# Optimization experiments

Measured on AMD Instinct MI355X. Metric: run time of the kernel, lower is better.

Reference implementation:

```python
import math
import jax, jax.numpy as jnp
import numpy as np

B, S, H = 2, 2048, 1024
NH = 16
HD = H // NH            # 64
ROT = int(HD * 0.25)    # 16
QKV_SLOTS = 1024
PROJ_SLOTS = 1024
FFN_SLOTS = 4096
EPS = 1e-5


def gelu_l2_norm(x, axis=-1):
    # F.gelu (exact erf) then L2-normalize and rescale by sqrt(dim)
    g = jax.nn.gelu(x, approximate=False)
    n = jnp.linalg.norm(g, ord=2, axis=axis, keepdims=True)
    return g / n * math.sqrt(g.shape[axis])


def layer_norm(x, w, b):
    mu = jnp.mean(x, axis=-1, keepdims=True)
    var = jnp.mean(jnp.square(x - mu), axis=-1, keepdims=True)
    return (x - mu) * jax.lax.rsqrt(var + EPS) * w + b


def pattention(x, key_tok, val_tok):
    # [.., in] @ [slots, in]^T -> [.., slots]; NOTE: scale MULTIPLIES (as in source)
    aw = jnp.einsum('bsh,ph->bsp', x, key_tok) * math.sqrt(x.shape[-1])
    aw = gelu_l2_norm(aw, axis=-1)
    return jnp.einsum('bsp,pd->bsd', aw, val_tok)


def rotary_cos_sin(seq_len, rot_dim, base=10000.0):
    inv_freq = 1.0 / (base ** (jnp.arange(0, rot_dim, 2, dtype=jnp.float32) / rot_dim))
    t = jnp.arange(seq_len, dtype=jnp.float32)
    freqs = jnp.einsum('s,d->sd', t, inv_freq)           # [S, rot/2]
    emb = jnp.concatenate([freqs, freqs], axis=-1)       # [S, rot]
    return jnp.cos(emb), jnp.sin(emb)


def rotate_half(x):
    x1, x2 = jnp.split(x, 2, axis=-1)
    return jnp.concatenate([-x2, x1], axis=-1)


def setup_inputs() -> dict:
    key = jax.random.key(0)
    ks = jax.random.split(key, 12)
    p = lambda k, shape: jax.random.normal(k, shape, dtype=jnp.float32) * 0.02
    return {
        'x': jax.random.normal(ks[0], (B, S, H), dtype=jnp.float32),
        'ln1_w': jnp.ones((H,), jnp.float32), 'ln1_b': jnp.zeros((H,), jnp.float32),
        'ln2_w': jnp.ones((H,), jnp.float32), 'ln2_b': jnp.zeros((H,), jnp.float32),
        'q_key': p(ks[1], (QKV_SLOTS, H)), 'q_val': p(ks[2], (QKV_SLOTS, H)),
        'k_key': p(ks[3], (QKV_SLOTS, H)), 'k_val': p(ks[4], (QKV_SLOTS, H)),
        'v_key': p(ks[5], (QKV_SLOTS, H)), 'v_val': p(ks[6], (QKV_SLOTS, H)),
        'proj_key': p(ks[7], (PROJ_SLOTS, H)), 'proj_val': p(ks[8], (PROJ_SLOTS, H)),
        'ffn_key': p(ks[9], (FFN_SLOTS, H)), 'ffn_val': p(ks[10], (FFN_SLOTS, H)),
    }


def reference(x, ln1_w, ln1_b, ln2_w, ln2_b, q_key, q_val, k_key, k_val,
              v_key, v_val, proj_key, proj_val, ffn_key, ffn_val):
    residual = x
    xn = layer_norm(x, ln1_w, ln1_b)
    q = pattention(xn, q_key, q_val).reshape(B, S, NH, HD)
    k = pattention(xn, k_key, k_val).reshape(B, S, NH, HD)
    v = pattention(xn, v_key, v_val).reshape(B, S, NH, HD)

    cos, sin = rotary_cos_sin(S, ROT)          # [S, ROT]
    cos = cos[None, :, None, :]
    sin = sin[None, :, None, :]
    q_rot, q_pass = q[..., :ROT], q[..., ROT:]
    k_rot, k_pass = k[..., :ROT], k[..., ROT:]
    q_rot = q_rot * cos + rotate_half(q_rot) * sin
    k_rot = k_rot * cos + rotate_half(k_rot) * sin
    q = jnp.concatenate([q_rot, q_pass], axis=-1).transpose(0, 2, 1, 3)  # [B,NH,S,HD]
    k = jnp.concatenate([k_rot, k_pass], axis=-1).transpose(0, 2, 1, 3)
    v = v.transpose(0, 2, 1, 3)

    scale = math.sqrt(HD)
    causal = jnp.triu(jnp.ones((S, S), dtype=bool), k=1)
    attn_mask = jnp.where(causal, jnp.float32(-10000.0), jnp.float32(0.0))
    aw = jnp.einsum('bhqd,bhkd->bhqk', q, k) / scale + attn_mask
    aw = gelu_l2_norm(aw, axis=-1)
    o = jnp.einsum('bhqk,bhkd->bhqd', aw, v)
    o = o.transpose(0, 2, 1, 3).reshape(B, S, H)

    x = residual + pattention(o, proj_key, proj_val)
    residual = x
    x = residual + pattention(layer_norm(x, ln2_w, ln2_b), ffn_key, ffn_val)
    return x
```

## Files before the change

kernel.cpp:

```cpp
#include <hip/hip_runtime.h>

typedef __bf16 bf16x8 __attribute__((ext_vector_type(8)));
typedef float f32x4 __attribute__((ext_vector_type(4)));
typedef unsigned short u16;

__device__ __forceinline__ float b2f(u16 u) {
  union { unsigned int i; float f; } v; v.i = ((unsigned int)u) << 16; return v.f;
}
__device__ __forceinline__ u16 f2b(float f) {
  union { float f; unsigned int i; } v; v.f = f;
  unsigned int x = v.i;
  x += 0x7fffu + ((x >> 16) & 1u);
  return (u16)(x >> 16);
}
__device__ __forceinline__ float gelu_f(float x) {
  float x2 = x * x;
  float p = x * (1.5957691216f + 0.0713548162f * x2);
  float e = __expf(p);
  float r = __builtin_amdgcn_rcpf(1.0f + e);
  return x - x * r;
}
__device__ __forceinline__ void async16(const u16* g, u16* l) {
  __builtin_amdgcn_global_load_lds(
      (const __attribute__((address_space(1))) void*)g,
      (__attribute__((address_space(3))) void*)l, 16, 0, 0);
}
__device__ __forceinline__ void swz(int& bn, int& bm, int& bz) {
  int gx = (int)gridDim.x, gy = (int)gridDim.y;
  int flat = (int)(blockIdx.x + gridDim.x * (blockIdx.y + gridDim.y * blockIdx.z));
  int seq = flat >> 3;
  int nbm = gy >> 3;
  bm = (flat & 7) * nbm + seq % nbm;
  int rest = seq / nbm;
  bn = rest % gx;
  bz = rest / gx;
}

union U4 { uint4 u; u16 s[8]; };

__global__ __launch_bounds__(256) void zero_kernel(float* __restrict__ p, int n) {
  int i = blockIdx.x * 256 + threadIdx.x;
  if (i < n) p[i] = 0.f;
}

__global__ __launch_bounds__(256) void cvt8_kernel(
    const float* __restrict__ qk, const float* __restrict__ kk,
    const float* __restrict__ vk, const float* __restrict__ pk,
    const float* __restrict__ fk, u16* __restrict__ w) {
  int z = blockIdx.y;
  const float* in = (z == 0) ? qk : (z == 1) ? kk : (z == 2) ? vk : (z == 3) ? pk
                    : fk + (size_t)(z - 4) * 4194304 / 4 * 4;
  if (z >= 4) in = fk + (size_t)(z - 4) * 1048576 * 4 / 4;
  in = (z == 0) ? qk : (z == 1) ? kk : (z == 2) ? vk : (z == 3) ? pk
       : fk + (size_t)(z - 4) * 1048576;
  u16* o = w + (size_t)z * 1048576;
  int i = blockIdx.x * 256 + threadIdx.x;
  float4 f = ((const float4*)in)[i];
  ushort4 s;
  s.x = f2b(f.x); s.y = f2b(f.y); s.z = f2b(f.z); s.w = f2b(f.w);
  ((ushort4*)o)[i] = s;
}

__global__ __launch_bounds__(256) void cvtT_kernel(const float* __restrict__ in,
                                                   u16* __restrict__ out, int R, int Cn) {
  __shared__ float t[32][33];
  int bc = blockIdx.x, br = blockIdx.y;
  int tid = threadIdx.x;
  int r = tid >> 5, c = tid & 31;
  #pragma unroll
  for (int i = 0; i < 4; ++i)
    t[r + i * 8][c] = in[(size_t)(br * 32 + r + i * 8) * Cn + bc * 32 + c];
  __syncthreads();
  #pragma unroll
  for (int i = 0; i < 4; ++i)
    out[(size_t)(bc * 32 + r + i * 8) * R + br * 32 + c] = f2b(t[c][r + i * 8]);
}
__global__ __launch_bounds__(256) void cvtT4_kernel(
    const float* __restrict__ a, const float* __restrict__ b,
    const float* __restrict__ c, const float* __restrict__ d,
    u16* __restrict__ out) {
  __shared__ float t[32][33];
  int z = blockIdx.z;
  const float* in = (z == 0) ? a : (z == 1) ? b : (z == 2) ? c : d;
  u16* o = out + (size_t)z * 1048576;
  int bc = blockIdx.x, br = blockIdx.y;
  int tid = threadIdx.x;
  int r = tid >> 5, cc = tid & 31;
  #pragma unroll
  for (int i = 0; i < 4; ++i)
    t[r + i * 8][cc] = in[(size_t)(br * 32 + r + i * 8) * 1024 + bc * 32 + cc];
  __syncthreads();
  #pragma unroll
  for (int i = 0; i < 4; ++i)
    o[(size_t)(bc * 32 + r + i * 8) * 1024 + br * 32 + cc] = f2b(t[cc][r + i * 8]);
}

__global__ __launch_bounds__(256) void ln_kernel(const float* __restrict__ x,
    const float* __restrict__ w, const float* __restrict__ b, u16* __restrict__ out) {
  int wv = threadIdx.x >> 6, lane = threadIdx.x & 63;
  int row = blockIdx.x * 4 + wv;
  const float* xr = x + (size_t)row * 1024;
  float4 v[4];
  float s = 0.f, s2 = 0.f;
  #pragma unroll
  for (int i = 0; i < 4; ++i) {
    v[i] = ((const float4*)xr)[lane + 64 * i];
    s += v[i].x + v[i].y + v[i].z + v[i].w;
    s2 += v[i].x * v[i].x + v[i].y * v[i].y + v[i].z * v[i].z + v[i].w * v[i].w;
  }
  #pragma unroll
  for (int m = 1; m < 64; m <<= 1) { s += __shfl_xor(s, m); s2 += __shfl_xor(s2, m); }
  float mu = s * (1.0f / 1024.0f);
  float inv = rsqrtf(s2 * (1.0f / 1024.0f) - mu * mu + 1e-5f);
  u16* orow = out + (size_t)row * 1024;
  #pragma unroll
  for (int i = 0; i < 4; ++i) {
    int c = (lane + 64 * i) * 4;
    ushort4 o;
    o.x = f2b((v[i].x - mu) * inv * w[c]     + b[c]);
    o.y = f2b((v[i].y - mu) * inv * w[c + 1] + b[c + 1]);
    o.z = f2b((v[i].z - mu) * inv * w[c + 2] + b[c + 2]);
    o.w = f2b((v[i].w - mu) * inv * w[c + 3] + b[c + 3]);
    ((ushort4*)orow)[lane + 64 * i] = o;
  }
}

template <int TM>
__global__ __launch_bounds__(256) void gemm_key(
    const u16* __restrict__ A, size_t sAz,
    const u16* __restrict__ B, size_t sBz,
    u16* __restrict__ C, size_t sCz,
    float* __restrict__ ssqb, size_t sSz,
    int N, int K, float alpha) {
  constexpr int AI = TM / 32;
  __shared__ __align__(16) u16 As[2][TM * 32];
  __shared__ __align__(16) u16 Bs[2][128 * 32];
  int bn, bm, bz;
  swz(bn, bm, bz);
  const u16* Ab = A + (size_t)bz * sAz + (size_t)bm * TM * K;
  const u16* Bb = B + (size_t)bz * sBz + (size_t)bn * 128 * K;
  int tid = threadIdx.x, lane = tid & 63, wv = tid >> 6;
  int quad = lane >> 4, l16 = lane & 15;
  int lr = lane >> 2, lc = (lane & 3) * 8;
  int wm = wv >> 1, wn = wv & 1;
  int RB = wm * (TM / 2), CB = wn * 64;
  f32x4 zero = {0.f, 0.f, 0.f, 0.f};
  f32x4 acc[AI][4];
  #pragma unroll
  for (int i = 0; i < AI; ++i)
    #pragma unroll
    for (int j = 0; j < 4; ++j) acc[i][j] = zero;
  #pragma unroll
  for (int t = 0; t < TM / 64; ++t) {
    int ia = wv * (TM / 64) + t;
    async16(Ab + (size_t)(ia * 16 + lr) * K + lc, &As[0][ia * 512]);
  }
  #pragma unroll
  for (int t = 0; t < 2; ++t) {
    int ib = wv * 2 + t;
    async16(Bb + (size_t)(ib * 16 + lr) * K + lc, &Bs[0][ib * 512]);
  }
  for (int k0 = 0, cur = 0; k0 < K; k0 += 32, cur ^= 1) {
    __syncthreads();
    if (k0 + 32 < K) {
      #pragma unroll
      for (int t = 0; t < TM / 64; ++t) {
        int ia = wv * (TM / 64) + t;
        async16(Ab + (size_t)(ia * 16 + lr) * K + k0 + 32 + lc, &As[cur ^ 1][ia * 512]);
      }
      #pragma unroll
      for (int t = 0; t < 2; ++t) {
        int ib = wv * 2 + t;
        async16(Bb + (size_t)(ib * 16 + lr) * K + k0 + 32 + lc, &Bs[cur ^ 1][ib * 512]);
      }
    }
    bf16x8 af[AI], bf[4];
    #pragma unroll
    for (int i = 0; i < AI; ++i)
      af[i] = *(const bf16x8*)&As[cur][(RB + i * 16 + l16) * 32 + quad * 8];
    #pragma unroll
    for (int j = 0; j < 4; ++j)
      bf[j] = *(const bf16x8*)&Bs[cur][(CB + j * 16 + l16) * 32 + quad * 8];
    #pragma unroll
    for (int i = 0; i < AI; ++i)
      #pragma unroll
      for (int j = 0; j < 4; ++j)
        acc[i][j] = __builtin_amdgcn_mfma_f32_16x16x32_bf16(af[i], bf[j], acc[i][j], 0, 0, 0);
  }
  #pragma unroll
  for (int i = 0; i < AI; ++i) {
    int rbase = bm * TM + RB + i * 16 + quad * 4;
    float srow[4] = {0.f, 0.f, 0.f, 0.f};
    #pragma unroll
    for (int j = 0; j < 4; ++j) {
      int c = bn * 128 + CB + j * 16 + l16;
      #pragma unroll
      for (int reg = 0; reg < 4; ++reg) {
        float g = gelu_f(acc[i][j][reg] * alpha);
        srow[reg] += g * g;
        C[(size_t)bz * sCz + (size_t)(rbase + reg) * N + c] = f2b(g);
      }
    }
    #pragma unroll
    for (int reg = 0; reg < 4; ++reg) {
      float s = srow[reg];
      s += __shfl_xor(s, 1); s += __shfl_xor(s, 2);
      s += __shfl_xor(s, 4); s += __shfl_xor(s, 8);
      if (l16 == 0) atomicAdd(&ssqb[bz * sSz + rbase + reg], s);
    }
  }
}

template <int TM, int MODE>
__global__ __launch_bounds__(256) void gemm_val(
    const u16* __restrict__ A, size_t sAz,
    const u16* __restrict__ B, size_t sBz,
    void* __restrict__ C, size_t sCz,
    const float* __restrict__ ssqb, size_t sSz,
    int N, int K, int kzs, int klen, float sqrtP, const float* __restrict__ res) {
  constexpr int AI = TM / 32;
  __shared__ __align__(16) u16 As[2][TM * 32];
  __shared__ __align__(16) u16 Bs[2][128 * 32];
  int bn, bm, bz;
  swz(bn, bm, bz);
  const u16* Ab = A + (size_t)bz * sAz + (size_t)bm * TM * K;
  const u16* Bb = B + (size_t)bz * sBz + (size_t)bn * 128 * K;
  int tid = threadIdx.x, lane = tid & 63, wv = tid >> 6;
  int quad = lane >> 4, l16 = lane & 15;
  int lr = lane >> 2, lc = (lane & 3) * 8;
  int wm = wv >> 1, wn = wv & 1;
  int RB = wm * (TM / 2), CB = wn * 64;
  f32x4 zero = {0.f, 0.f, 0.f, 0.f};
  f32x4 acc[AI][4];
  #pragma unroll
  for (int i = 0; i < AI; ++i)
    #pragma unroll
    for (int j = 0; j < 4; ++j) acc[i][j] = zero;
  int kb0 = bz * kzs;
  #pragma unroll
  for (int t = 0; t < TM / 64; ++t) {
    int ia = wv * (TM / 64) + t;
    async16(Ab + (size_t)(ia * 16 + lr) * K + kb0 + lc, &As[0][ia * 512]);
  }
  #pragma unroll
  for (int t = 0; t < 2; ++t) {
    int ib = wv * 2 + t;
    async16(Bb + (size_t)(ib * 16 + lr) * K + kb0 + lc, &Bs[0][ib * 512]);
  }
  for (int k0 = kb0, cur = 0; k0 < kb0 + klen; k0 += 32, cur ^= 1) {
    __syncthreads();
    if (k0 + 32 < kb0 + klen) {
      #pragma unroll
      for (int t = 0; t < TM / 64; ++t) {
        int ia = wv * (TM / 64) + t;
        async16(Ab + (size_t)(ia * 16 + lr) * K + k0 + 32 + lc, &As[cur ^ 1][ia * 512]);
      }
      #pragma unroll
      for (int t = 0; t < 2; ++t) {
        int ib = wv * 2 + t;
        async16(Bb + (size_t)(ib * 16 + lr) * K + k0 + 32 + lc, &Bs[cur ^ 1][ib * 512]);
      }
    }
    bf16x8 af[AI], bf[4];
    #pragma unroll
    for (int i = 0; i < AI; ++i)
      af[i] = *(const bf16x8*)&As[cur][(RB + i * 16 + l16) * 32 + quad * 8];
    #pragma unroll
    for (int j = 0; j < 4; ++j)
      bf[j] = *(const bf16x8*)&Bs[cur][(CB + j * 16 + l16) * 32 + quad * 8];
    #pragma unroll
    for (int i = 0; i < AI; ++i)
      #pragma unroll
      for (int j = 0; j < 4; ++j)
        acc[i][j] = __builtin_amdgcn_mfma_f32_16x16x32_bf16(af[i], bf[j], acc[i][j], 0, 0, 0);
  }
  #pragma unroll
  for (int i = 0; i < AI; ++i) {
    int rbase = bm * TM + RB + i * 16 + quad * 4;
    float sc[4];
    if (MODE < 2) {
      #pragma unroll
      for (int reg = 0; reg < 4; ++reg)
        sc[reg] = sqrtP * rsqrtf(ssqb[bz * sSz + rbase + reg]);
    }
    #pragma unroll
    for (int j = 0; j < 4; ++j) {
      int c = bn * 128 + CB + j * 16 + l16;
      #pragma unroll
      for (int reg = 0; reg < 4; ++reg) {
        float v = acc[i][j][reg];
        size_t idx = (size_t)(rbase + reg) * N + c;
        if (MODE == 0) {
          ((u16*)C)[(size_t)bz * sCz + idx] = f2b(v * sc[reg]);
        } else if (MODE == 1) {
          ((float*)C)[idx] = v * sc[reg] + res[idx];
        } else {
          ((float*)C)[(size_t)bz * sCz + idx] = v;
        }
      }
    }
  }
}

__global__ __launch_bounds__(256) void rotary_kernel(u16* __restrict__ qb, u16* __restrict__ kb) {
  const float F[8] = {1.f, 0.31622776601683794f, 0.1f, 0.03162277660168379f,
                      0.01f, 0.0031622776601683794f, 0.001f, 0.00031622776601683794f};
  int t = blockIdx.x * 256 + threadIdx.x;
  int m = t >> 4;
  int h = t & 15;
  int s = m & 2047;
  u16* qp = qb + (size_t)m * 1024 + h * 64;
  u16* kp = kb + (size_t)m * 1024 + h * 64;
  float q[16], k[16];
  #pragma unroll
  for (int d = 0; d < 16; ++d) { q[d] = b2f(qp[d]); k[d] = b2f(kp[d]); }
  #pragma unroll
  for (int i = 0; i < 8; ++i) {
    float ang = (float)s * F[i];
    float c = cosf(ang), sn = sinf(ang);
    qp[i]     = f2b(q[i] * c - q[i + 8] * sn);
    qp[i + 8] = f2b(q[i + 8] * c + q[i] * sn);
    kp[i]     = f2b(k[i] * c - k[i + 8] * sn);
    kp[i + 8] = f2b(k[i + 8] * c + k[i] * sn);
  }
}

__global__ __launch_bounds__(256) void vt_kernel(const u16* __restrict__ vb,
                                                 u16* __restrict__ vT) {
  __shared__ __align__(16) u16 T[64][72];
  int st = blockIdx.x, bh = blockIdx.y;
  int b = bh >> 4, h = bh & 15;
  int tid = threadIdx.x;
  #pragma unroll
  for (int i = 0; i < 2; ++i) {
    int l = tid + 256 * i;
    int s = l >> 3, dc = l & 7;
    *(uint4*)&T[s][dc * 8] =
        *(const uint4*)(vb + (size_t)(b * 2048 + st * 64 + s) * 1024 + h * 64 + dc * 8);
  }
  __syncthreads();
  #pragma unroll
  for (int i = 0; i < 2; ++i) {
    int l = tid + 256 * i;
    int d = l >> 3, scid = l & 7;
    U4 u;
    #pragma unroll
    for (int j = 0; j < 8; ++j) u.s[j] = T[scid * 8 + j][d];
    *(uint4*)(vT + ((size_t)bh * 64 + d) * 2048 + st * 64 + scid * 8) = u.u;
  }
}

__global__ __launch_bounds__(256) void attn_kernel(
    const u16* __restrict__ qb, const u16* __restrict__ kb,
    const u16* __restrict__ vT, u16* __restrict__ ob) {
  __shared__ __align__(16) u16 Qs[64 * 64];
  __shared__ __align__(16) u16 Ks[2][64 * 64];
  __shared__ __align__(16) u16 Vts[2][64 * 64];
  __shared__ __align__(16) u16 Sg[64 * 72];
  int bh = blockIdx.x;
  int qt = 31 - (int)blockIdx.y;
  int b = bh >> 4, h = bh & 15;
  const u16* qp = qb + (size_t)b * 2048 * 1024 + h * 64;
  const u16* kp = kb + (size_t)b * 2048 * 1024 + h * 64;
  const u16* vp = vT + (size_t)bh * 64 * 2048;
  int tid = threadIdx.x, lane = tid & 63, wv = tid >> 6;
  int quad = lane >> 4, l16 = lane & 15;
  int lr8 = lane >> 3, lc8 = (lane & 7) * 8;
  int MR = wv * 16;
  int nkt = qt + 1;
  #pragma unroll
  for (int t = 0; t < 2; ++t) {
    int idx = wv * 2 + t;
    async16(qp + (size_t)(qt * 64 + idx * 8 + lr8) * 1024 + lc8, &Qs[idx * 512]);
    async16(kp + (size_t)(idx * 8 + lr8) * 1024 + lc8, &Ks[0][idx * 512]);
    async16(vp + (size_t)(idx * 8 + lr8) * 2048 + lc8, &Vts[0][idx * 512]);
  }
  f32x4 zero = {0.f, 0.f, 0.f, 0.f};
  f32x4 oacc[4];
  float ssqr[4] = {0.f, 0.f, 0.f, 0.f};
  #pragma unroll
  for (int dn = 0; dn < 4; ++dn) oacc[dn] = zero;
  for (int kt = 0, cur = 0; kt < nkt; ++kt, cur ^= 1) {
    __syncthreads();
    if (kt + 1 < nkt) {
      #pragma unroll
      for (int t = 0; t < 2; ++t) {
        int idx = wv * 2 + t;
        async16(kp + (size_t)((kt + 1) * 64 + idx * 8 + lr8) * 1024 + lc8, &Ks[cur ^ 1][idx * 512]);
        async16(vp + (size_t)(idx * 8 + lr8) * 2048 + (kt + 1) * 64 + lc8, &Vts[cur ^ 1][idx * 512]);
      }
    }
    bf16x8 a0 = *(const bf16x8*)&Qs[(MR + l16) * 64 + quad * 8];
    bf16x8 a1 = *(const bf16x8*)&Qs[(MR + l16) * 64 + 32 + quad * 8];
    bool dg = (kt == qt);
    #pragma unroll
    for (int sn = 0; sn < 4; ++sn) {
      bf16x8 b0 = *(const bf16x8*)&Ks[cur][(sn * 16 + l16) * 64 + quad * 8];
      bf16x8 b1 = *(const bf16x8*)&Ks[cur][(sn * 16 + l16) * 64 + 32 + quad * 8];
      f32x4 s = zero;
      s = __builtin_amdgcn_mfma_f32_16x16x32_bf16(a0, b0, s, 0, 0, 0);
      s = __builtin_amdgcn_mfma_f32_16x16x32_bf16(a1, b1, s, 0, 0, 0);
      int srow = MR + quad * 4;
      int kcol = sn * 16 + l16;
      #pragma unroll
      for (int reg = 0; reg < 4; ++reg) {
        float gl = gelu_f(s[reg] * 0.125f);
        if (dg && kcol > srow + reg) gl = 0.f;
        ssqr[reg] += gl * gl;
        Sg[(srow + reg) * 72 + kcol] = f2b(gl);
      }
    }
    bf16x8 p0 = *(const bf16x8*)&Sg[(MR + l16) * 72 + quad * 8];
    bf16x8 p1 = *(const bf16x8*)&Sg[(MR + l16) * 72 + 32 + quad * 8];
    #pragma unroll
    for (int dn = 0; dn < 4; ++dn) {
      bf16x8 v0 = *(const bf16x8*)&Vts[cur][(dn * 16 + l16) * 64 + quad * 8];
      bf16x8 v1 = *(const bf16x8*)&Vts[cur][(dn * 16 + l16) * 64 + 32 + quad * 8];
      oacc[dn] = __builtin_amdgcn_mfma_f32_16x16x32_bf16(p0, v0, oacc[dn], 0, 0, 0);
      oacc[dn] = __builtin_amdgcn_mfma_f32_16x16x32_bf16(p1, v1, oacc[dn], 0, 0, 0);
    }
  }
  float sc[4];
  #pragma unroll
  for (int reg = 0; reg < 4; ++reg) {
    float s = ssqr[reg];
    s += __shfl_xor(s, 1); s += __shfl_xor(s, 2);
    s += __shfl_xor(s, 4); s += __shfl_xor(s, 8);
    sc[reg] = 45.254834f * rsqrtf(s);
  }
  #pragma unroll
  for (int dn = 0; dn < 4; ++dn)
    #pragma unroll
    for (int reg = 0; reg < 4; ++reg) {
      int row = qt * 64 + MR + quad * 4 + reg;
      int col = h * 64 + dn * 16 + l16;
      ob[(size_t)(b * 2048 + row) * 1024 + col] = f2b(oacc[dn][reg] * sc[reg]);
    }
}

__global__ __launch_bounds__(256) void fin_kernel(
    const float* __restrict__ p0, const float* __restrict__ p1,
    const float* __restrict__ x1, const float* __restrict__ ssqf,
    float* __restrict__ out) {
  int row = blockIdx.x, t = threadIdx.x;
  float s = 64.0f * rsqrtf(ssqf[row]);
  size_t base = (size_t)row * 1024 + t * 4;
  float4 a = *(const float4*)(p0 + base);
  float4 b = *(const float4*)(p1 + base);
  float4 r = *(const float4*)(x1 + base);
  float4 o;
  o.x = r.x + s * (a.x + b.x); o.y = r.y + s * (a.y + b.y);
  o.z = r.z + s * (a.z + b.z); o.w = r.w + s * (a.w + b.w);
  *(float4*)(out + base) = o;
}

extern "C" void kernel_launch(void* const* d_in, const int* in_sizes, int n_in,
                              void* d_out, int out_size, void* d_ws, size_t ws_size,
                              hipStream_t stream) {
  const float* x    = (const float*)d_in[0];
  const float* ln1w = (const float*)d_in[1];
  const float* ln1b = (const float*)d_in[2];
  const float* ln2w = (const float*)d_in[3];
  const float* ln2b = (const float*)d_in[4];
  const float* qk   = (const float*)d_in[5];
  const float* qv   = (const float*)d_in[6];
  const float* kk   = (const float*)d_in[7];
  const float* kv   = (const float*)d_in[8];
  const float* vk   = (const float*)d_in[9];
  const float* vv   = (const float*)d_in[10];
  const float* pk   = (const float*)d_in[11];
  const float* pv   = (const float*)d_in[12];
  const float* fk   = (const float*)d_in[13];
  const float* fv   = (const float*)d_in[14];
  float* out = (float*)d_out;

  const size_t M1 = 1048576;
  u16* w = (u16*)d_ws;
  u16* wkeys  = w;
  u16* wpk    = w + 3 * M1;
  u16* wfk    = w + 4 * M1;
  u16* wvalsT = w + 8 * M1;
  u16* wpvT   = w + 11 * M1;
  u16* wfvT   = w + 12 * M1;
  u16* xn     = w + 16 * M1;
  u16* gq     = w + 20 * M1;
  u16* ob     = w + 20 * M1;
  u16* gp     = w + 24 * M1;
  u16* gf     = w + 20 * M1;
  u16* qb     = w + 36 * M1;
  u16* kb     = w + 40 * M1;
  u16* vb     = w + 44 * M1;
  u16* vT     = w + 48 * M1;
  float* ssq_qkv  = (float*)(w + 48 * M1);
  float* ssq_proj = ssq_qkv + 12288;
  float* ssq_ffn  = ssq_qkv + 16384;
  float* x1 = (float*)(w + 52 * M1);
  float* p0 = (float*)w;
  float* p1 = (float*)(w + 36 * M1);

  dim3 blk(256);
  zero_kernel<<<80, blk, 0, stream>>>(ssq_qkv, 20480);
  cvt8_kernel<<<dim3(1024, 8), blk, 0, stream>>>(qk, kk, vk, pk, fk, w);
  cvtT4_kernel<<<dim3(32, 32, 4), blk, 0, stream>>>(qv, kv, vv, pv, wvalsT);
  cvtT_kernel<<<dim3(32, 128), blk, 0, stream>>>(fv, wfvT, 4096, 1024);

  ln_kernel<<<1024, blk, 0, stream>>>(x, ln1w, ln1b, xn);
  gemm_key<128><<<dim3(8, 32, 3), blk, 0, stream>>>(
      xn, 0, wkeys, M1, gq, 4 * M1, ssq_qkv, 4096, 1024, 1024, 32.0f);
  gemm_val<128, 0><<<dim3(8, 32, 3), blk, 0, stream>>>(
      gq, 4 * M1, wvalsT, M1, qb, 4 * M1, ssq_qkv, 4096, 1024, 1024, 0, 1024, 32.0f, nullptr);

  rotary_kernel<<<256, blk, 0, stream>>>(qb, kb);
  vt_kernel<<<dim3(32, 32), blk, 0, stream>>>(vb, vT);
  attn_kernel<<<dim3(32, 32), blk, 0, stream>>>(qb, kb, vT, ob);
  zero_kernel<<<32, blk, 0, stream>>>(ssq_proj, 8192);

  gemm_key<64><<<dim3(8, 64, 1), blk, 0, stream>>>(
      ob, 0, wpk, 0, gp, 0, ssq_proj, 0, 1024, 1024, 32.0f);
  gemm_val<64, 1><<<dim3(8, 64, 1), blk, 0, stream>>>(
      gp, 0, wpvT, 0, x1, 0, ssq_proj, 0, 1024, 1024, 0, 1024, 32.0f, x);

  ln_kernel<<<1024, blk, 0, stream>>>(x1, ln2w, ln2b, xn);
  gemm_key<128><<<dim3(32, 32, 1), blk, 0, stream>>>(
      xn, 0, wfk, 0, gf, 0, ssq_ffn, 0, 4096, 1024, 32.0f);
  gemm_val<128, 2><<<dim3(8, 32, 2), blk, 0, stream>>>(
      gf, 0, wfvT, 0, p0, 18 * M1, ssq_ffn, 0, 1024, 4096, 2048, 2048, 0.0f, nullptr);
  fin_kernel<<<4096, blk, 0, stream>>>(p0, p1, x1, ssq_ffn, out);
}
```

Measured before the change: 470.5 us.

## Fuse rotary into QKV epilogue, keep attention probs in registers, merge setup kernels

Applies the rotary embedding inside the Q/K value-GEMM epilogue, using a lane shuffle to fetch the paired element, so the separate rotary kernel and its extra pass over Q and K go away. The attention kernel now computes S transposed (K as the A operand) so the GELU'd probabilities land directly in the register layout the PV MFMA needs. This removes the shared-memory staging buffer Sg and its round trip, and V^T is permuted to match. The zero-fill and weight-conversion kernels are merged into fewer launches. The risk is in the new lane-layout assumptions (the shuffle pairing, the vT permutation and the mask index), which could silently produce wrong results.

```diff
diff --git a/kernel.cpp b/kernel.cpp
--- a/kernel.cpp
+++ b/kernel.cpp
@@ -37,52 +37,41 @@
 }
 
 union U4 { uint4 u; u16 s[8]; };
-
-__global__ __launch_bounds__(256) void zero_kernel(float* __restrict__ p, int n) {
-  int i = blockIdx.x * 256 + threadIdx.x;
-  if (i < n) p[i] = 0.f;
-}
-
-__global__ __launch_bounds__(256) void cvt8_kernel(
+union PF { bf16x8 v; u16 s[8]; };
+
+__global__ __launch_bounds__(256) void cvt9_kernel(
     const float* __restrict__ qk, const float* __restrict__ kk,
     const float* __restrict__ vk, const float* __restrict__ pk,
-    const float* __restrict__ fk, u16* __restrict__ w) {
+    const float* __restrict__ fk, u16* __restrict__ w, float* __restrict__ ssqz) {
   int z = blockIdx.y;
+  int i = blockIdx.x * 256 + threadIdx.x;
+  if (z == 8) {
+    if (i < 20480) ssqz[i] = 0.f;
+    return;
+  }
   const float* in = (z == 0) ? qk : (z == 1) ? kk : (z == 2) ? vk : (z == 3) ? pk
-                    : fk + (size_t)(z - 4) * 4194304 / 4 * 4;
-  if (z >= 4) in = fk + (size_t)(z - 4) * 1048576 * 4 / 4;
-  in = (z == 0) ? qk : (z == 1) ? kk : (z == 2) ? vk : (z == 3) ? pk
-       : fk + (size_t)(z - 4) * 1048576;
+                    : fk + (size_t)(z - 4) * 1048576;
   u16* o = w + (size_t)z * 1048576;
-  int i = blockIdx.x * 256 + threadIdx.x;
   float4 f = ((const float4*)in)[i];
   ushort4 s;
   s.x = f2b(f.x); s.y = f2b(f.y); s.z = f2b(f.z); s.w = f2b(f.w);
   ((ushort4*)o)[i] = s;
 }
 
-__global__ __launch_bounds__(256) void cvtT_kernel(const float* __restrict__ in,
-                                                   u16* __restrict__ out, int R, int Cn) {
-  __shared__ float t[32][33];
-  int bc = blockIdx.x, br = blockIdx.y;
-  int tid = threadIdx.x;
-  int r = tid >> 5, c = tid & 31;
-  #pragma unroll
-  for (int i = 0; i < 4; ++i)
-    t[r + i * 8][c] = in[(size_t)(br * 32 + r + i * 8) * Cn + bc * 32 + c];
-  __syncthreads();
-  #pragma unroll
-  for (int i = 0; i < 4; ++i)
-    out[(size_t)(bc * 32 + r + i * 8) * R + br * 32 + c] = f2b(t[c][r + i * 8]);
-}
-__global__ __launch_bounds__(256) void cvtT4_kernel(
-    const float* __restrict__ a, const float* __restrict__ b,
-    const float* __restrict__ c, const float* __restrict__ d,
-    u16* __restrict__ out) {
+__global__ __launch_bounds__(256) void cvtT8_kernel(
+    const float* __restrict__ qv, const float* __restrict__ kv,
+    const float* __restrict__ vv, const float* __restrict__ pv,
+    const float* __restrict__ fv, u16* __restrict__ valsT, u16* __restrict__ fvT) {
   __shared__ float t[32][33];
   int z = blockIdx.z;
-  const float* in = (z == 0) ? a : (z == 1) ? b : (z == 2) ? c : d;
-  u16* o = out + (size_t)z * 1048576;
+  const float* in; u16* o; int Rout, rowoff;
+  if (z < 4) {
+    in = (z == 0) ? qv : (z == 1) ? kv : (z == 2) ? vv : pv;
+    o = valsT + (size_t)z * 1048576; Rout = 1024; rowoff = 0;
+  } else {
+    in = fv + (size_t)(z - 4) * 1048576;
+    o = fvT; Rout = 4096; rowoff = (z - 4) * 1024;
+  }
   int bc = blockIdx.x, br = blockIdx.y;
   int tid = threadIdx.x;
   int r = tid >> 5, cc = tid & 31;
@@ -92,7 +81,7 @@
   __syncthreads();
   #pragma unroll
   for (int i = 0; i < 4; ++i)
-    o[(size_t)(bc * 32 + r + i * 8) * 1024 + br * 32 + cc] = f2b(t[cc][r + i * 8]);
+    o[(size_t)(bc * 32 + r + i * 8) * Rout + rowoff + br * 32 + cc] = f2b(t[cc][r + i * 8]);
 }
 
 __global__ __launch_bounds__(256) void ln_kernel(const float* __restrict__ x,
@@ -211,7 +200,7 @@
   }
 }
 
-template <int TM, int MODE>
+template <int TM, int MODE, bool ROT>
 __global__ __launch_bounds__(256) void gemm_val(
     const u16* __restrict__ A, size_t sAz,
     const u16* __restrict__ B, size_t sBz,
@@ -291,7 +280,18 @@
         float v = acc[i][j][reg];
         size_t idx = (size_t)(rbase + reg) * N + c;
         if (MODE == 0) {
-          ((u16*)C)[(size_t)bz * sCz + idx] = f2b(v * sc[reg]);
+          float vs = v * sc[reg];
+          if (ROT && j == 0) {
+            float prt = __shfl_xor(vs, 8);
+            if (bz < 2) {
+              int seq = (rbase + reg) & 2047;
+              float fr = exp2f((float)(l16 & 7) * -1.66096404744368f);
+              float ang = (float)seq * fr;
+              float c_ = __cosf(ang), s_ = __sinf(ang);
+              vs = (l16 < 8) ? (vs * c_ - prt * s_) : (vs * c_ + prt * s_);
+            }
+          }
+          ((u16*)C)[(size_t)bz * sCz + idx] = f2b(vs);
         } else if (MODE == 1) {
           ((float*)C)[idx] = v * sc[reg] + res[idx];
         } else {
@@ -299,29 +299,6 @@
         }
       }
     }
-  }
-}
-
-__global__ __launch_bounds__(256) void rotary_kernel(u16* __restrict__ qb, u16* __restrict__ kb) {
-  const float F[8] = {1.f, 0.31622776601683794f, 0.1f, 0.03162277660168379f,
-                      0.01f, 0.0031622776601683794f, 0.001f, 0.00031622776601683794f};
-  int t = blockIdx.x * 256 + threadIdx.x;
-  int m = t >> 4;
-  int h = t & 15;
-  int s = m & 2047;
-  u16* qp = qb + (size_t)m * 1024 + h * 64;
-  u16* kp = kb + (size_t)m * 1024 + h * 64;
-  float q[16], k[16];
-  #pragma unroll
-  for (int d = 0; d < 16; ++d) { q[d] = b2f(qp[d]); k[d] = b2f(kp[d]); }
-  #pragma unroll
-  for (int i = 0; i < 8; ++i) {
-    float ang = (float)s * F[i];
-    float c = cosf(ang), sn = sinf(ang);
-    qp[i]     = f2b(q[i] * c - q[i + 8] * sn);
-    qp[i + 8] = f2b(q[i + 8] * c + q[i] * sn);
-    kp[i]     = f2b(k[i] * c - k[i + 8] * sn);
-    kp[i + 8] = f2b(k[i + 8] * c + k[i] * sn);
   }
 }
 
@@ -343,9 +320,12 @@
   for (int i = 0; i < 2; ++i) {
     int l = tid + 256 * i;
     int d = l >> 3, scid = l & 7;
+    int blk = (scid >> 2) * 32;
+    int qq = (scid & 3) * 4;
     U4 u;
     #pragma unroll
-    for (int j = 0; j < 8; ++j) u.s[j] = T[scid * 8 + j][d];
+    for (int j = 0; j < 8; ++j)
+      u.s[j] = T[blk + (j >> 2) * 16 + qq + (j & 3)][d];
     *(uint4*)(vT + ((size_t)bh * 64 + d) * 2048 + st * 64 + scid * 8) = u.u;
   }
 }
@@ -356,7 +336,6 @@
   __shared__ __align__(16) u16 Qs[64 * 64];
   __shared__ __align__(16) u16 Ks[2][64 * 64];
   __shared__ __align__(16) u16 Vts[2][64 * 64];
-  __shared__ __align__(16) u16 Sg[64 * 72];
   int bh = blockIdx.x;
   int qt = 31 - (int)blockIdx.y;
   int b = bh >> 4, h = bh & 15;
@@ -377,11 +356,16 @@
   }
   f32x4 zero = {0.f, 0.f, 0.f, 0.f};
   f32x4 oacc[4];
-  float ssqr[4] = {0.f, 0.f, 0.f, 0.f};
   #pragma unroll
   for (int dn = 0; dn < 4; ++dn) oacc[dn] = zero;
+  float ssql = 0.f;
+  bf16x8 bq0 = {}, bq1 = {};
   for (int kt = 0, cur = 0; kt < nkt; ++kt, cur ^= 1) {
     __syncthreads();
+    if (kt == 0) {
+      bq0 = *(const bf16x8*)&Qs[(MR + l16) * 64 + quad * 8];
+      bq1 = *(const bf16x8*)&Qs[(MR + l16) * 64 + 32 + quad * 8];
+    }
     if (kt + 1 < nkt) {
       #pragma unroll
       for (int t = 0; t < 2; ++t) {
@@ -390,51 +374,44 @@
         async16(vp + (size_t)(idx * 8 + lr8) * 2048 + (kt + 1) * 64 + lc8, &Vts[cur ^ 1][idx * 512]);
       }
     }
-    bf16x8 a0 = *(const bf16x8*)&Qs[(MR + l16) * 64 + quad * 8];
-    bf16x8 a1 = *(const bf16x8*)&Qs[(MR + l16) * 64 + 32 + quad * 8];
     bool dg = (kt == qt);
     #pragma unroll
-    for (int sn = 0; sn < 4; ++sn) {
-      bf16x8 b0 = *(const bf16x8*)&Ks[cur][(sn * 16 + l16) * 64 + quad * 8];
-      bf16x8 b1 = *(const bf16x8*)&Ks[cur][(sn * 16 + l16) * 64 + 32 + quad * 8];
-      f32x4 s = zero;
-      s = __builtin_amdgcn_mfma_f32_16x16x32_bf16(a0, b0, s, 0, 0, 0);
-      s = __builtin_amdgcn_mfma_f32_16x16x32_bf16(a1, b1, s, 0, 0, 0);
-      int srow = MR + quad * 4;
-      int kcol = sn * 16 + l16;
-      #pragma unroll
-      for (int reg = 0; reg < 4; ++reg) {
-        float gl = gelu_f(s[reg] * 0.125f);
-        if (dg && kcol > srow + reg) gl = 0.f;
-        ssqr[reg] += gl * gl;
-        Sg[(srow + reg) * 72 + kcol] = f2b(gl);
-      }
-    }
-    bf16x8 p0 = *(const bf16x8*)&Sg[(MR + l16) * 72 + quad * 8];
-    bf16x8 p1 = *(const bf16x8*)&Sg[(MR + l16) * 72 + 32 + quad * 8];
-    #pragma unroll
-    for (int dn = 0; dn < 4; ++dn) {
-      bf16x8 v0 = *(const bf16x8*)&Vts[cur][(dn * 16 + l16) * 64 + quad * 8];
-      bf16x8 v1 = *(const bf16x8*)&Vts[cur][(dn * 16 + l16) * 64 + 32 + quad * 8];
-      oacc[dn] = __builtin_amdgcn_mfma_f32_16x16x32_bf16(p0, v0, oacc[dn], 0, 0, 0);
-      oacc[dn] = __builtin_amdgcn_mfma_f32_16x16x32_bf16(p1, v1, oacc[dn], 0, 0, 0);
-    }
-  }
-  float sc[4];
-  #pragma unroll
-  for (int reg = 0; reg < 4; ++reg) {
-    float s = ssqr[reg];
-    s += __shfl_xor(s, 1); s += __shfl_xor(s, 2);
-    s += __shfl_xor(s, 4); s += __shfl_xor(s, 8);
-    sc[reg] = 45.254834f * rsqrtf(s);
-  }
+    for (int kc = 0; kc < 2; ++kc) {
+      PF pf;
+      #pragma unroll
+      for (int snh = 0; snh < 2; ++snh) {
+        int sn = kc * 2 + snh;
+        bf16x8 ak0 = *(const bf16x8*)&Ks[cur][(sn * 16 + l16) * 64 + quad * 8];
+        bf16x8 ak1 = *(const bf16x8*)&Ks[cur][(sn * 16 + l16) * 64 + 32 + quad * 8];
+        f32x4 st = zero;
+        st = __builtin_amdgcn_mfma_f32_16x16x32_bf16(ak0, bq0, st, 0, 0, 0);
+        st = __builtin_amdgcn_mfma_f32_16x16x32_bf16(ak1, bq1, st, 0, 0, 0);
+        #pragma unroll
+        for (int r = 0; r < 4; ++r) {
+          float gl = gelu_f(st[r] * 0.125f);
+          if (dg && (sn * 16 + quad * 4 + r > MR + l16)) gl = 0.f;
+          ssql += gl * gl;
+          pf.s[snh * 4 + r] = f2b(gl);
+        }
+      }
+      #pragma unroll
+      for (int dn = 0; dn < 4; ++dn) {
+        bf16x8 bv = *(const bf16x8*)&Vts[cur][(dn * 16 + l16) * 64 + kc * 32 + quad * 8];
+        oacc[dn] = __builtin_amdgcn_mfma_f32_16x16x32_bf16(pf.v, bv, oacc[dn], 0, 0, 0);
+      }
+    }
+  }
+  ssql += __shfl_xor(ssql, 16);
+  ssql += __shfl_xor(ssql, 32);
+  float sc = 45.254834f * rsqrtf(ssql);
   #pragma unroll
   for (int dn = 0; dn < 4; ++dn)
     #pragma unroll
-    for (int reg = 0; reg < 4; ++reg) {
-      int row = qt * 64 + MR + quad * 4 + reg;
+    for (int r = 0; r < 4; ++r) {
+      float scr = __shfl(sc, quad * 4 + r);
+      int row = qt * 64 + MR + quad * 4 + r;
       int col = h * 64 + dn * 16 + l16;
-      ob[(size_t)(b * 2048 + row) * 1024 + col] = f2b(oacc[dn][reg] * sc[reg]);
+      ob[(size_t)(b * 2048 + row) * 1024 + col] = f2b(oacc[dn][r] * scr);
     }
 }
 
@@ -485,12 +462,12 @@
   u16* xn     = w + 16 * M1;
   u16* gq     = w + 20 * M1;
   u16* ob     = w + 20 * M1;
-  u16* gp     = w + 24 * M1;
+  u16* vT     = w + 24 * M1;
+  u16* gp     = w + 28 * M1;
   u16* gf     = w + 20 * M1;
   u16* qb     = w + 36 * M1;
   u16* kb     = w + 40 * M1;
   u16* vb     = w + 44 * M1;
-  u16* vT     = w + 48 * M1;
   float* ssq_qkv  = (float*)(w + 48 * M1);
   float* ssq_proj = ssq_qkv + 12288;
   float* ssq_ffn  = ssq_qkv + 16384;
@@ -499,31 +476,27 @@
   float* p1 = (float*)(w + 36 * M1);
 
   dim3 blk(256);
-  zero_kernel<<<80, blk, 0, stream>>>(ssq_qkv, 20480);
-  cvt8_kernel<<<dim3(1024, 8), blk, 0, stream>>>(qk, kk, vk, pk, fk, w);
-  cvtT4_kernel<<<dim3(32, 32, 4), blk, 0, stream>>>(qv, kv, vv, pv, wvalsT);
-  cvtT_kernel<<<dim3(32, 128), blk, 0, stream>>>(fv, wfvT, 4096, 1024);
+  cvt9_kernel<<<dim3(1024, 9), blk, 0, stream>>>(qk, kk, vk, pk, fk, w, ssq_qkv);
+  cvtT8_kernel<<<dim3(32, 32, 8), blk, 0, stream>>>(qv, kv, vv, pv, fv, wvalsT, wfvT);
 
   ln_kernel<<<1024, blk, 0, stream>>>(x, ln1w, ln1b, xn);
   gemm_key<128><<<dim3(8, 32, 3), blk, 0, stream>>>(
       xn, 0, wkeys, M1, gq, 4 * M1, ssq_qkv, 4096, 1024, 1024, 32.0f);
-  gemm_val<128, 0><<<dim3(8, 32, 3), blk, 0, stream>>>(
+  gemm_val<128, 0, true><<<dim3(8, 32, 3), blk, 0, stream>>>(
       gq, 4 * M1, wvalsT, M1, qb, 4 * M1, ssq_qkv, 4096, 1024, 1024, 0, 1024, 32.0f, nullptr);
 
-  rotary_kernel<<<256, blk, 0, stream>>>(qb, kb);
   vt_kernel<<<dim3(32, 32), blk, 0, stream>>>(vb, vT);
   attn_kernel<<<dim3(32, 32), blk, 0, stream>>>(qb, kb, vT, ob);
-  zero_kernel<<<32, blk, 0, stream>>>(ssq_proj, 8192);
 
   gemm_key<64><<<dim3(8, 64, 1), blk, 0, stream>>>(
       ob, 0, wpk, 0, gp, 0, ssq_proj, 0, 1024, 1024, 32.0f);
-  gemm_val<64, 1><<<dim3(8, 64, 1), blk, 0, stream>>>(
+  gemm_val<64, 1, false><<<dim3(8, 64, 1), blk, 0, stream>>>(
       gp, 0, wpvT, 0, x1, 0, ssq_proj, 0, 1024, 1024, 0, 1024, 32.0f, x);
 
   ln_kernel<<<1024, blk, 0, stream>>>(x1, ln2w, ln2b, xn);
   gemm_key<128><<<dim3(32, 32, 1), blk, 0, stream>>>(
       xn, 0, wfk, 0, gf, 0, ssq_ffn, 0, 4096, 1024, 32.0f);
-  gemm_val<128, 2><<<dim3(8, 32, 2), blk, 0, stream>>>(
+  gemm_val<128, 2, false><<<dim3(8, 32, 2), blk, 0, stream>>>(
       gf, 0, wfvT, 0, p0, 18 * M1, ssq_ffn, 0, 1024, 4096, 2048, 2048, 0.0f, nullptr);
   fin_kernel<<<4096, blk, 0, stream>>>(p0, p1, x1, ssq_ffn, out);
 }
```

New measurement: 445.1 us. -5.4%, faster.
